# Performance work log

Hardware: AMD Instinct MI355X
Metric: run time of the kernel (lower is better)

Reference implementation:

```python
import jax, jax.numpy as jnp
import numpy as np
import math

B = 256          # batch size
D = 128          # input_size (embed dim)
N = 500000       # output_size == num_samples (memory bank rows)
K = 2048         # num_negative_samples
T = 0.07         # temperature
MOM = 0.5        # momentum
EPS = 1e-07


def _l2norm(x):
    return x / jnp.linalg.norm(x, axis=-1, keepdims=True)


def setup_inputs() -> dict:
    key = jax.random.key(0)
    k1, k2, k3, k4, k5, k6 = jax.random.split(key, 6)
    stdv = 1.0 / math.sqrt(D / 3.0)
    memory_v1 = jax.random.uniform(k1, (N, D), dtype=jnp.float32) * (2 * stdv) - stdv
    memory_v2 = jax.random.uniform(k2, (N, D), dtype=jnp.float32) * (2 * stdv) - stdv
    # embeds come out of an L2-normalization module in the original pipeline
    student_embed = _l2norm(jax.random.normal(k3, (B, D), dtype=jnp.float32))
    teacher_embed = _l2norm(jax.random.normal(k4, (B, D), dtype=jnp.float32))
    pos_idx = jax.random.randint(k5, (B,), 0, N, dtype=jnp.int64)
    contrast_idx = jax.random.randint(k6, (B, K + 1), 0, N, dtype=jnp.int64)
    contrast_idx = contrast_idx.at[:, 0].set(pos_idx)  # column 0 holds the positive
    return {
        'student_embed': student_embed,
        'teacher_embed': teacher_embed,
        'memory_v1': memory_v1,
        'memory_v2': memory_v2,
        'pos_idx': pos_idx,
        'contrast_idx': contrast_idx,
    }


def _contrast_loss(x):
    # x: [B, K+1] normalized exp-similarities; column 0 is the positive
    m = x.shape[1] - 1
    pn = 1.0 / float(N)  # num_samples
    noise = m * pn + EPS
    p_pos = x[:, 0]
    log_d1 = jnp.log(p_pos / (p_pos + noise))
    p_neg = x[:, 1:]
    log_d0 = jnp.log((m * pn) / (p_neg + noise))
    return -(log_d1.sum() + log_d0.sum()) / x.shape[0]


def reference(student_embed, teacher_embed, memory_v1, memory_v2, pos_idx, contrast_idx):
    output_size = memory_v1.shape[0]
    # gather [B, K+1, D] rows from each bank (detached in original)
    w1 = jax.lax.stop_gradient(memory_v1[contrast_idx])
    w2 = jax.lax.stop_gradient(memory_v2[contrast_idx])
    # per-sample bmm + exp/div  (teacher scored against v1 bank, student against v2)
    out_v2 = jnp.exp(jnp.einsum('bkd,bd->bk', w1, teacher_embed) / T)
    out_v1 = jnp.exp(jnp.einsum('bkd,bd->bk', w2, student_embed) / T)
    # first-call normalization constants (treated as constants thereafter)
    z_v1 = jax.lax.stop_gradient(out_v1.mean() * output_size)
    z_v2 = jax.lax.stop_gradient(out_v2.mean() * output_size)
    out_v1 = out_v1 / z_v1
    out_v2 = out_v2 / z_v2
    # momentum-weighted renormalize-and-scatter memory update (no_grad)
    s = jax.lax.stop_gradient(student_embed)
    t = jax.lax.stop_gradient(teacher_embed)
    l_pos = memory_v1[pos_idx] * MOM + s * (1.0 - MOM)
    updated_v1 = l_pos / jnp.sqrt((l_pos ** 2).sum(1, keepdims=True))
    new_memory_v1 = memory_v1.at[pos_idx].set(updated_v1)
    ab_pos = memory_v2[pos_idx] * MOM + t * (1.0 - MOM)
    updated_v2 = ab_pos / jnp.sqrt((ab_pos ** 2).sum(1, keepdims=True))
    new_memory_v2 = memory_v2.at[pos_idx].set(updated_v2)
    loss = _contrast_loss(out_v1) + _contrast_loss(out_v2)
    return loss, new_memory_v1, new_memory_v2
```

## Files before the change

### kernel.cpp

```cpp
#include <hip/hip_runtime.h>
#include <math.h>

namespace {
constexpr int kB = 256;
constexpr int kD = 128;
constexpr int kN = 500000;
constexpr int kKC = 2049;
constexpr int kNPair = kB * kKC;
constexpr float kTInv = 1.0f / 0.07f;
constexpr float kMom = 0.5f;
constexpr int kRB = 256;
constexpr long long kM = (long long)kN * kD;
constexpr long long kTot = 2 * kM;
constexpr int kChunk = 2048;
constexpr int kNB1 = (kN + kChunk - 1) / kChunk;
constexpr int kRows = 64;
constexpr int kTPB = (kN + kRows - 1) / kRows;
constexpr int kTiles = 2 * kTPB;
constexpr int kLdsStride = 132;
constexpr int kTilesPerBlock = 8;
constexpr int kGrid3 = (kTiles + kTilesPerBlock - 1) / kTilesPerBlock;
}


__global__ __launch_bounds__(256) void zero2_kernel(int* __restrict__ A, int* __restrict__ cur)
{
    int i = blockIdx.x * 256 + threadIdx.x;
    if (i < kN) { A[i] = 0; cur[i] = 0; }
}

__global__ __launch_bounds__(256) void hist_kernel(const int* __restrict__ cidx, int* __restrict__ A)
{
    int i = blockIdx.x * 256 + threadIdx.x;
    if (i < kNPair) atomicAdd(&A[cidx[i]], 1);
}

__global__ __launch_bounds__(256) void scan1_kernel(const int* __restrict__ A, int* __restrict__ bsum)
{
    long long base = (long long)blockIdx.x * kChunk;
    int t = threadIdx.x;
    int s = 0;
    #pragma unroll
    for (int j = 0; j < 8; ++j) {
        long long i = base + t * 8 + j;
        if (i < kN) s += A[i];
    }
    __shared__ int lds[256];
    lds[t] = s; __syncthreads();
    for (int st = 128; st > 0; st >>= 1) {
        if (t < st) lds[t] += lds[t + st];
        __syncthreads();
    }
    if (t == 0) bsum[blockIdx.x] = lds[0];
}

__global__ __launch_bounds__(256) void scan2_kernel(
    const int* __restrict__ bsum, int* __restrict__ bpre, int* __restrict__ offs)
{
    int t = threadIdx.x;
    int v = (t < kNB1) ? bsum[t] : 0;
    __shared__ int lds[256];
    lds[t] = v; __syncthreads();
    for (int st = 1; st < 256; st <<= 1) {
        int add = (t >= st) ? lds[t - st] : 0;
        __syncthreads();
        lds[t] += add;
        __syncthreads();
    }
    if (t < kNB1) bpre[t] = lds[t] - v;
    if (t == kNB1 - 1) offs[kN] = lds[t];
}

__global__ __launch_bounds__(256) void scan3_kernel(
    const int* __restrict__ A, const int* __restrict__ bpre, int* __restrict__ offs)
{
    int t = threadIdx.x;
    long long base = (long long)blockIdx.x * kChunk;
    int c[8]; int s = 0;
    #pragma unroll
    for (int j = 0; j < 8; ++j) {
        long long i = base + t * 8 + j;
        c[j] = (i < kN) ? A[i] : 0;
        s += c[j];
    }
    __shared__ int lds[256];
    lds[t] = s; __syncthreads();
    for (int st = 1; st < 256; st <<= 1) {
        int add = (t >= st) ? lds[t - st] : 0;
        __syncthreads();
        lds[t] += add;
        __syncthreads();
    }
    int excl = lds[t] - s + bpre[blockIdx.x];
    #pragma unroll
    for (int j = 0; j < 8; ++j) {
        long long i = base + t * 8 + j;
        if (i < kN) { offs[i] = excl; excl += c[j]; }
    }
}

__global__ __launch_bounds__(256) void scatter_kernel(
    const int* __restrict__ cidx, const int* __restrict__ offs,
    int* __restrict__ cur, int* __restrict__ sorted)
{
    int p = blockIdx.x * 256 + threadIdx.x;
    if (p < kNPair) {
        int r = cidx[p];
        int pos = offs[r] + atomicAdd(&cur[r], 1);
        sorted[pos] = p;
    }
}

__global__ __launch_bounds__(256) void fused3_kernel(
    const float* __restrict__ mem1, const float* __restrict__ mem2,
    const float* __restrict__ teacher, const float* __restrict__ student,
    const int* __restrict__ offs, const int* __restrict__ sorted,
    const int* __restrict__ cidx,
    float* __restrict__ out, float* __restrict__ e2, float* __restrict__ e1)
{
    __shared__ float tile[kRows * kLdsStride];
    const int tid = threadIdx.x;
    const int lane = tid & 63;
    const int w = tid >> 6;
    float4* ov = reinterpret_cast<float4*>(out);

    if (blockIdx.x == 0 && tid == 0) out[kTot] = mem2[kM - 1];

    int T0 = blockIdx.x * kTilesPerBlock;
    int T1 = T0 + kTilesPerBlock; if (T1 > kTiles) T1 = kTiles;
    for (int T = T0; T < T1; ++T) {
        int bk = (T >= kTPB) ? 1 : 0;
        int tt = T - bk * kTPB;
        int r0 = tt * kRows;
        int R  = kN - r0; if (R > kRows) R = kRows;

        if (w * 16 < R) {
            const float4* bank4 = reinterpret_cast<const float4*>(bk ? mem2 : mem1);
            long long chunk = (long long)r0 * kD + w * 2048;
            long long cb4   = chunk >> 2;
            long long base4 = (((long long)bk * kM) + chunk) >> 2;
            float4 v[8];
            #pragma unroll
            for (int i = 0; i < 8; ++i) v[i] = bank4[cb4 + i * 64 + lane];
            float carry = 0.f;
            long long gg = (long long)bk * kM + chunk - 1;
            if (gg >= 0) carry = (gg < kM) ? mem1[gg] : mem2[gg - kM];
            #pragma unroll
            for (int i = 0; i < 8; ++i) {
                float4 cur = v[i];
                int lr  = w * 16 + i * 2 + (lane >> 5);
                int col = (lane & 31) * 4;
                *reinterpret_cast<float4*>(&tile[lr * kLdsStride + col]) = cur;
                float pw = __shfl_up(cur.w, 1);
                if (lane == 0) pw = carry;
                carry = __shfl(cur.w, 63);
                long long k4 = base4 + i * 64 + lane;
                if (k4 != 0) {
                    ov[k4] = make_float4(pw, cur.x, cur.y, cur.z);
                } else {
                    out[1] = cur.x; out[2] = cur.y; out[3] = cur.z;
                }
            }
        }
        __syncthreads();

        int o0  = offs[r0];
        int cnt = offs[r0 + R] - o0;
        const float* emb = bk ? student : teacher;
        float* ep = bk ? e1 : e2;
        for (int t = tid; t < cnt; t += 256) {
            int p  = sorted[o0 + t];
            int lr = cidx[p] - r0;
            unsigned b = (unsigned)p / (unsigned)kKC;
            const float4* er = reinterpret_cast<const float4*>(emb + (long long)b * kD);
            const float* row = &tile[lr * kLdsStride];
            float ax = 0.f, ay = 0.f, az = 0.f, aw = 0.f;
            #pragma unroll 8
            for (int kk = 0; kk < 32; ++kk) {
                float4 rv = *reinterpret_cast<const float4*>(&row[kk * 4]);
                float4 ev = er[kk];
                ax += rv.x * ev.x; ay += rv.y * ev.y;
                az += rv.z * ev.z; aw += rv.w * ev.w;
            }
            ep[p] = __expf((ax + ay + az + aw) * kTInv);
        }
        __syncthreads();
    }
}


__global__ __launch_bounds__(256) void dots_kernel(
    const float* __restrict__ mem1, const float* __restrict__ mem2,
    const float* __restrict__ teacher, const float* __restrict__ student,
    const int* __restrict__ cidx,
    float* __restrict__ e2, float* __restrict__ e1)
{
    int gtid = blockIdx.x * 256 + threadIdx.x;
    int wave = gtid >> 6;
    int lane = threadIdx.x & 63;
    if (wave >= kNPair) return;
    int b = wave / kKC;
    long long row = (long long)cidx[wave] * kD;
    const float2 m1 = *reinterpret_cast<const float2*>(mem1 + row + lane * 2);
    const float2 m2 = *reinterpret_cast<const float2*>(mem2 + row + lane * 2);
    const float2 tv = *reinterpret_cast<const float2*>(teacher + b * kD + lane * 2);
    const float2 sv = *reinterpret_cast<const float2*>(student + b * kD + lane * 2);
    float d1 = m1.x * tv.x + m1.y * tv.y;
    float d2 = m2.x * sv.x + m2.y * sv.y;
    #pragma unroll
    for (int off = 32; off > 0; off >>= 1) {
        d1 += __shfl_xor(d1, off);
        d2 += __shfl_xor(d2, off);
    }
    if (lane == 0) {
        e2[wave] = __expf(d1 * kTInv);
        e1[wave] = __expf(d2 * kTInv);
    }
}

__global__ __launch_bounds__(256) void copy_kernel(
    const float* __restrict__ mem1, const float* __restrict__ mem2,
    float* __restrict__ out)
{
    const long long NV4 = (kTot + 1) / 4;
    const long long KS  = kM / 4;
    const float4* m1v = reinterpret_cast<const float4*>(mem1);
    const float4* m2v = reinterpret_cast<const float4*>(mem2);
    float4* ov = reinterpret_cast<float4*>(out);
    long long stride = (long long)gridDim.x * 256;
    for (long long k = (long long)blockIdx.x * 256 + threadIdx.x; k < NV4; k += stride) {
        if (k == 0) {
            out[1] = mem1[0]; out[2] = mem1[1]; out[3] = mem1[2];
            out[kTot] = mem2[kM - 1];
            continue;
        }
        float4 r;
        if (k < KS) {
            float4 a = m1v[k - 1];
            float4 b = m1v[k];
            r = make_float4(a.w, b.x, b.y, b.z);
        } else if (k == KS) {
            r = make_float4(mem1[kM - 1], mem2[0], mem2[1], mem2[2]);
        } else {
            float4 a = m2v[k - KS - 1];
            float4 b = m2v[k - KS];
            r = make_float4(a.w, b.x, b.y, b.z);
        }
        ov[k] = r;
    }
}


__global__ __launch_bounds__(256) void sums_kernel(
    const float* __restrict__ e2, const float* __restrict__ e1,
    float* __restrict__ p2, float* __restrict__ p1)
{
    __shared__ float s2[256], s1[256];
    float a2 = 0.f, a1 = 0.f;
    for (int i = blockIdx.x * 256 + threadIdx.x; i < kNPair; i += 256 * kRB) {
        a2 += e2[i];
        a1 += e1[i];
    }
    s2[threadIdx.x] = a2; s1[threadIdx.x] = a1;
    __syncthreads();
    for (int st = 128; st > 0; st >>= 1) {
        if ((int)threadIdx.x < st) {
            s2[threadIdx.x] += s2[threadIdx.x + st];
            s1[threadIdx.x] += s1[threadIdx.x + st];
        }
        __syncthreads();
    }
    if (threadIdx.x == 0) { p2[blockIdx.x] = s2[0]; p1[blockIdx.x] = s1[0]; }
}

__global__ __launch_bounds__(256) void z_kernel(
    const float* __restrict__ p2, const float* __restrict__ p1, float* __restrict__ z)
{
    __shared__ float s2[256], s1[256];
    s2[threadIdx.x] = p2[threadIdx.x];
    s1[threadIdx.x] = p1[threadIdx.x];
    __syncthreads();
    for (int st = 128; st > 0; st >>= 1) {
        if ((int)threadIdx.x < st) {
            s2[threadIdx.x] += s2[threadIdx.x + st];
            s1[threadIdx.x] += s1[threadIdx.x + st];
        }
        __syncthreads();
    }
    if (threadIdx.x == 0) {
        const float scale = (float)kN / (float)kNPair;
        z[0] = s2[0] * scale;
        z[1] = s1[0] * scale;
    }
}

__global__ __launch_bounds__(256) void lossp_kernel(
    const float* __restrict__ e2, const float* __restrict__ e1,
    const float* __restrict__ z, float* __restrict__ lp)
{
    const float mpn = 2048.0f / 500000.0f;
    const float noise = mpn + 1e-7f;
    const float iz2 = 1.0f / z[0];
    const float iz1 = 1.0f / z[1];
    float acc = 0.f;
    for (int i = blockIdx.x * 256 + threadIdx.x; i < kNPair; i += 256 * kRB) {
        int k = i % kKC;
        float x2 = e2[i] * iz2;
        float x1 = e1[i] * iz1;
        if (k == 0) {
            acc += __logf(x2 / (x2 + noise)) + __logf(x1 / (x1 + noise));
        } else {
            acc += __logf(mpn / (x2 + noise)) + __logf(mpn / (x1 + noise));
        }
    }
    __shared__ float s[256];
    s[threadIdx.x] = acc;
    __syncthreads();
    for (int st = 128; st > 0; st >>= 1) {
        if ((int)threadIdx.x < st) s[threadIdx.x] += s[threadIdx.x + st];
        __syncthreads();
    }
    if (threadIdx.x == 0) lp[blockIdx.x] = s[0];
}

__global__ __launch_bounds__(256) void final_kernel(
    const float* __restrict__ lp, float* __restrict__ out)
{
    __shared__ float s[256];
    s[threadIdx.x] = lp[threadIdx.x];
    __syncthreads();
    for (int st = 128; st > 0; st >>= 1) {
        if ((int)threadIdx.x < st) s[threadIdx.x] += s[threadIdx.x + st];
        __syncthreads();
    }
    if (threadIdx.x == 0) out[0] = -s[0] / (float)kB;
}


__global__ __launch_bounds__(64) void update_kernel(
    const float* __restrict__ mem1, const float* __restrict__ mem2,
    const float* __restrict__ student, const float* __restrict__ teacher,
    const int* __restrict__ pos_idx,
    float* __restrict__ out1, float* __restrict__ out2)
{
    int b = blockIdx.x;
    int lane = threadIdx.x;
    int p = pos_idx[b];
    for (int b2 = b + 1; b2 < kB; ++b2)
        if (pos_idx[b2] == p) return;
    long long row = (long long)p * kD;
    float2 m1 = *reinterpret_cast<const float2*>(mem1 + row + lane * 2);
    float2 m2 = *reinterpret_cast<const float2*>(mem2 + row + lane * 2);
    float2 sv = *reinterpret_cast<const float2*>(student + b * kD + lane * 2);
    float2 tv = *reinterpret_cast<const float2*>(teacher + b * kD + lane * 2);
    float2 l1 = make_float2(m1.x * kMom + sv.x * (1.f - kMom),
                            m1.y * kMom + sv.y * (1.f - kMom));
    float2 l2 = make_float2(m2.x * kMom + tv.x * (1.f - kMom),
                            m2.y * kMom + tv.y * (1.f - kMom));
    float n1 = l1.x * l1.x + l1.y * l1.y;
    float n2 = l2.x * l2.x + l2.y * l2.y;
    #pragma unroll
    for (int off = 32; off > 0; off >>= 1) {
        n1 += __shfl_xor(n1, off);
        n2 += __shfl_xor(n2, off);
    }
    float i1 = 1.0f / sqrtf(n1);
    float i2 = 1.0f / sqrtf(n2);
    out1[row + lane * 2]     = l1.x * i1;
    out1[row + lane * 2 + 1] = l1.y * i1;
    out2[row + lane * 2]     = l2.x * i2;
    out2[row + lane * 2 + 1] = l2.y * i2;
}

extern "C" void kernel_launch(void* const* d_in, const int* in_sizes, int n_in,
                              void* d_out, int out_size, void* d_ws, size_t ws_size,
                              hipStream_t stream) {
    const float* student = (const float*)d_in[0];
    const float* teacher = (const float*)d_in[1];
    const float* mem1    = (const float*)d_in[2];
    const float* mem2    = (const float*)d_in[3];
    const int*   pos_idx = (const int*)d_in[4];
    const int*   cidx    = (const int*)d_in[5];

    float* out  = (float*)d_out;
    float* out1 = out + 1;
    float* out2 = out + 1 + kM;

    float* ws = (float*)d_ws;
    float* e2 = ws;
    float* e1 = e2 + kNPair;
    float* p2 = e1 + kNPair;
    float* p1 = p2 + kRB;
    float* zz = p1 + kRB;
    float* lp = zz + 2;
    int*   A      = (int*)(lp + kRB);
    int*   cur    = A + kN;
    int*   offs   = cur + kN;
    int*   bsum   = offs + kN + 1;
    int*   bpre   = bsum + kNB1;
    int*   sorted = bpre + kNB1;
    size_t need = (size_t)((char*)(sorted + kNPair) - (char*)d_ws);

    if (ws_size >= need) {
        zero2_kernel<<<(kN + 255) / 256, 256, 0, stream>>>(A, cur);
        hist_kernel<<<(kNPair + 255) / 256, 256, 0, stream>>>(cidx, A);
        scan1_kernel<<<kNB1, 256, 0, stream>>>(A, bsum);
        scan2_kernel<<<1, 256, 0, stream>>>(bsum, bpre, offs);
        scan3_kernel<<<kNB1, 256, 0, stream>>>(A, bpre, offs);
        scatter_kernel<<<(kNPair + 255) / 256, 256, 0, stream>>>(cidx, offs, cur, sorted);
        fused3_kernel<<<kGrid3, 256, 0, stream>>>(mem1, mem2, teacher, student,
                                                  offs, sorted, cidx, out, e2, e1);
    } else {
        int nblocks = (kNPair + 3) / 4;
        dots_kernel<<<nblocks, 256, 0, stream>>>(mem1, mem2, teacher, student, cidx, e2, e1);
        copy_kernel<<<2048, 256, 0, stream>>>(mem1, mem2, out);
    }

    sums_kernel<<<kRB, 256, 0, stream>>>(e2, e1, p2, p1);
    z_kernel<<<1, 256, 0, stream>>>(p2, p1, zz);
    lossp_kernel<<<kRB, 256, 0, stream>>>(e2, e1, zz, lp);
    final_kernel<<<1, 256, 0, stream>>>(lp, out);
    update_kernel<<<kB, 64, 0, stream>>>(mem1, mem2, student, teacher, pos_idx, out1, out2);
}
```

Measured before the change: 329.7 us.

## Make fused copy-and-dot kernel wave-independent with register double-buffered segment prefetch

The block-wide 64-row tiles shared by four waves are replaced by per-wave 16-row segments, each in its own LDS slice. The __syncthreads barriers are removed, and each wave now handles 8 consecutive segments. The next segment's bank data is loaded into registers while the current one is copied out and scored, so global loads overlap with the dot-product phase. This costs more registers per thread, and per-segment work can become unbalanced when few indices hit a segment.

New measurement: 361.4 us. 1.1x slower.

```diff
diff --git a/kernel.cpp b/kernel.cpp
--- a/kernel.cpp
+++ b/kernel.cpp
@@ -14,12 +14,14 @@
 constexpr long long kTot = 2 * kM;
 constexpr int kChunk = 2048;
 constexpr int kNB1 = (kN + kChunk - 1) / kChunk;
-constexpr int kRows = 64;
-constexpr int kTPB = (kN + kRows - 1) / kRows;
-constexpr int kTiles = 2 * kTPB;
 constexpr int kLdsStride = 132;
-constexpr int kTilesPerBlock = 8;
-constexpr int kGrid3 = (kTiles + kTilesPerBlock - 1) / kTilesPerBlock;
+constexpr int kSegRows = 16;
+constexpr int kSegFloats = kSegRows * kD;
+constexpr int kSegs = (int)(kTot / kSegFloats);
+constexpr int kSegsB1 = kSegs / 2;
+constexpr int kSPW = 8;
+constexpr int kWaves5 = (kSegs + kSPW - 1) / kSPW;
+constexpr int kBlocks5 = (kWaves5 + 3) / 4;
 }
 
 
@@ -111,69 +113,84 @@
     }
 }
 
-__global__ __launch_bounds__(256) void fused3_kernel(
+__global__ __launch_bounds__(256) void fused5_kernel(
     const float* __restrict__ mem1, const float* __restrict__ mem2,
     const float* __restrict__ teacher, const float* __restrict__ student,
     const int* __restrict__ offs, const int* __restrict__ sorted,
     const int* __restrict__ cidx,
     float* __restrict__ out, float* __restrict__ e2, float* __restrict__ e1)
 {
-    __shared__ float tile[kRows * kLdsStride];
+    __shared__ float tile[4][kSegRows * kLdsStride];
     const int tid = threadIdx.x;
     const int lane = tid & 63;
     const int w = tid >> 6;
+    float* my = tile[w];
+
+    long long gw = (long long)blockIdx.x * 4 + w;
+    long long s0 = gw * kSPW;
+    if (s0 >= kSegs) return;
+    long long s1 = s0 + kSPW; if (s1 > kSegs) s1 = kSegs;
+
     float4* ov = reinterpret_cast<float4*>(out);
-
-    if (blockIdx.x == 0 && tid == 0) out[kTot] = mem2[kM - 1];
-
-    int T0 = blockIdx.x * kTilesPerBlock;
-    int T1 = T0 + kTilesPerBlock; if (T1 > kTiles) T1 = kTiles;
-    for (int T = T0; T < T1; ++T) {
-        int bk = (T >= kTPB) ? 1 : 0;
-        int tt = T - bk * kTPB;
-        int r0 = tt * kRows;
-        int R  = kN - r0; if (R > kRows) R = kRows;
-
-        if (w * 16 < R) {
-            const float4* bank4 = reinterpret_cast<const float4*>(bk ? mem2 : mem1);
-            long long chunk = (long long)r0 * kD + w * 2048;
-            long long cb4   = chunk >> 2;
-            long long base4 = (((long long)bk * kM) + chunk) >> 2;
-            float4 v[8];
+    const float4* m1v = reinterpret_cast<const float4*>(mem1);
+    const float4* m2v = reinterpret_cast<const float4*>(mem2);
+
+    if (gw == 0 && lane == 0) out[kTot] = mem2[kM - 1];
+
+    float carry = 0.f;
+    if (s0 > 0) {
+        long long g = s0 * kSegFloats - 1;
+        carry = (g < kM) ? mem1[g] : mem2[g - kM];
+    }
+
+    float4 va[8];
+    {
+        bool b1 = (s0 < kSegsB1);
+        long long lb4 = (b1 ? s0 : s0 - kSegsB1) * 8 * 64;
+        const float4* bp = b1 ? m1v : m2v;
+        #pragma unroll
+        for (int i = 0; i < 8; ++i) va[i] = bp[lb4 + i * 64 + lane];
+    }
+
+    for (long long s = s0; s < s1; ++s) {
+        float4 vb[8];
+        if (s + 1 < s1) {
+            bool nb1 = (s + 1 < kSegsB1);
+            long long lb4 = (nb1 ? (s + 1) : (s + 1 - kSegsB1)) * 8 * 64;
+            const float4* bp = nb1 ? m1v : m2v;
             #pragma unroll
-            for (int i = 0; i < 8; ++i) v[i] = bank4[cb4 + i * 64 + lane];
-            float carry = 0.f;
-            long long gg = (long long)bk * kM + chunk - 1;
-            if (gg >= 0) carry = (gg < kM) ? mem1[gg] : mem2[gg - kM];
-            #pragma unroll
-            for (int i = 0; i < 8; ++i) {
-                float4 cur = v[i];
-                int lr  = w * 16 + i * 2 + (lane >> 5);
-                int col = (lane & 31) * 4;
-                *reinterpret_cast<float4*>(&tile[lr * kLdsStride + col]) = cur;
-                float pw = __shfl_up(cur.w, 1);
-                if (lane == 0) pw = carry;
-                carry = __shfl(cur.w, 63);
-                long long k4 = base4 + i * 64 + lane;
-                if (k4 != 0) {
-                    ov[k4] = make_float4(pw, cur.x, cur.y, cur.z);
-                } else {
-                    out[1] = cur.x; out[2] = cur.y; out[3] = cur.z;
-                }
+            for (int i = 0; i < 8; ++i) vb[i] = bp[lb4 + i * 64 + lane];
+        }
+
+        long long j0 = s * 8;
+        #pragma unroll
+        for (int i = 0; i < 8; ++i) {
+            float4 cur = va[i];
+            int lr = i * 2 + (lane >> 5);
+            *reinterpret_cast<float4*>(&my[lr * kLdsStride + (lane & 31) * 4]) = cur;
+            float pw = __shfl_up(cur.w, 1);
+            if (lane == 0) pw = carry;
+            carry = __shfl(cur.w, 63);
+            long long k4 = (j0 + i) * 64 + lane;
+            if (k4 != 0) {
+                ov[k4] = make_float4(pw, cur.x, cur.y, cur.z);
+            } else {
+                out[1] = cur.x; out[2] = cur.y; out[3] = cur.z;
             }
         }
-        __syncthreads();
-
+
+        bool b1 = (s < kSegsB1);
+        int r0 = (int)((b1 ? s : s - kSegsB1) * kSegRows);
         int o0  = offs[r0];
-        int cnt = offs[r0 + R] - o0;
-        const float* emb = bk ? student : teacher;
-        float* ep = bk ? e1 : e2;
-        for (int t = tid; t < cnt; t += 256) {
+        int cnt = offs[r0 + kSegRows] - o0;
+        const float* emb = b1 ? teacher : student;
+        float* ep = b1 ? e2 : e1;
+        for (int t = lane; t < cnt; t += 64) {
             int p  = sorted[o0 + t];
             int lr = cidx[p] - r0;
-            unsigned b = (unsigned)p / (unsigned)kKC;
-            const float4* er = reinterpret_cast<const float4*>(emb + (long long)b * kD);
-            const float* row = &tile[lr * kLdsStride];
+            unsigned bb = (unsigned)p / (unsigned)kKC;
+            const float4* er = reinterpret_cast<const float4*>(emb + (long long)bb * kD);
+            const float* row = &my[lr * kLdsStride];
             float ax = 0.f, ay = 0.f, az = 0.f, aw = 0.f;
             #pragma unroll 8
             for (int kk = 0; kk < 32; ++kk) {
@@ -184,7 +201,9 @@
             }
             ep[p] = __expf((ax + ay + az + aw) * kTInv);
         }
-        __syncthreads();
+
+        #pragma unroll
+        for (int i = 0; i < 8; ++i) va[i] = vb[i];
     }
 }
 
@@ -408,8 +427,8 @@
         scan2_kernel<<<1, 256, 0, stream>>>(bsum, bpre, offs);
         scan3_kernel<<<kNB1, 256, 0, stream>>>(A, bpre, offs);
         scatter_kernel<<<(kNPair + 255) / 256, 256, 0, stream>>>(cidx, offs, cur, sorted);
-        fused3_kernel<<<kGrid3, 256, 0, stream>>>(mem1, mem2, teacher, student,
-                                                  offs, sorted, cidx, out, e2, e1);
+        fused5_kernel<<<kBlocks5, 256, 0, stream>>>(mem1, mem2, teacher, student,
+                                                    offs, sorted, cidx, out, e2, e1);
     } else {
         int nblocks = (kNPair + 3) / 4;
         dots_kernel<<<nblocks, 256, 0, stream>>>(mem1, mem2, teacher, student, cidx, e2, e1);
```

## Prefetch next tile's bank rows into registers while processing current tile

Applied to the files above, without the earlier changes.

The fused copy+dot kernel now double-buffers the global loads of the memory-bank tile. Loads for the next tile are issued into a second register array before the current tile is written to LDS and scored, so memory latency can overlap compute. The __syncthreads calls become explicit s_barrier plus sched_barrier so the compiler keeps the early loads. Out-of-range loads are clamped and stores are masked instead of skipping whole waves. This doubles the register footprint of the staging buffers, which may reduce occupancy.

New measurement: 396.0 us. +20.1%, slower.

```diff
diff --git a/kernel.cpp b/kernel.cpp
--- a/kernel.cpp
+++ b/kernel.cpp
@@ -19,7 +19,7 @@
 constexpr int kTiles = 2 * kTPB;
 constexpr int kLdsStride = 132;
 constexpr int kTilesPerBlock = 8;
-constexpr int kGrid3 = (kTiles + kTilesPerBlock - 1) / kTilesPerBlock;
+constexpr int kGrid6 = (kTiles + kTilesPerBlock - 1) / kTilesPerBlock;
 }
 
 
@@ -111,7 +111,7 @@
     }
 }
 
-__global__ __launch_bounds__(256) void fused3_kernel(
+__global__ __launch_bounds__(256) void fused6_kernel(
     const float* __restrict__ mem1, const float* __restrict__ mem2,
     const float* __restrict__ teacher, const float* __restrict__ student,
     const int* __restrict__ offs, const int* __restrict__ sorted,
@@ -126,43 +126,59 @@
 
     if (blockIdx.x == 0 && tid == 0) out[kTot] = mem2[kM - 1];
 
-    int T0 = blockIdx.x * kTilesPerBlock;
+    const int T0 = blockIdx.x * kTilesPerBlock;
     int T1 = T0 + kTilesPerBlock; if (T1 > kTiles) T1 = kTiles;
-    for (int T = T0; T < T1; ++T) {
+
+    auto issue = [&](float4 (&v)[8], int T) {
         int bk = (T >= kTPB) ? 1 : 0;
         int tt = T - bk * kTPB;
-        int r0 = tt * kRows;
-        int R  = kN - r0; if (R > kRows) R = kRows;
-
-        if (w * 16 < R) {
-            const float4* bank4 = reinterpret_cast<const float4*>(bk ? mem2 : mem1);
-            long long chunk = (long long)r0 * kD + w * 2048;
-            long long cb4   = chunk >> 2;
-            long long base4 = (((long long)bk * kM) + chunk) >> 2;
-            float4 v[8];
-            #pragma unroll
-            for (int i = 0; i < 8; ++i) v[i] = bank4[cb4 + i * 64 + lane];
-            float carry = 0.f;
-            long long gg = (long long)bk * kM + chunk - 1;
-            if (gg >= 0) carry = (gg < kM) ? mem1[gg] : mem2[gg - kM];
-            #pragma unroll
-            for (int i = 0; i < 8; ++i) {
-                float4 cur = v[i];
-                int lr  = w * 16 + i * 2 + (lane >> 5);
-                int col = (lane & 31) * 4;
-                *reinterpret_cast<float4*>(&tile[lr * kLdsStride + col]) = cur;
-                float pw = __shfl_up(cur.w, 1);
-                if (lane == 0) pw = carry;
-                carry = __shfl(cur.w, 63);
-                long long k4 = base4 + i * 64 + lane;
+        const float4* bank4 = reinterpret_cast<const float4*>(bk ? mem2 : mem1);
+        long long cb4 = ((long long)tt * kRows * kD + w * 2048) >> 2;
+        const long long maxv4 = kM / 4 - 1;
+        #pragma unroll
+        for (int i = 0; i < 8; ++i) {
+            long long e4 = cb4 + i * 64 + lane;
+            if (e4 > maxv4) e4 = maxv4;
+            v[i] = bank4[e4];
+        }
+    };
+
+    auto body = [&](float4 (&v)[8], float4 (&nxt)[8], int T, bool hasNext) {
+        if (hasNext) issue(nxt, T + 1);
+        __builtin_amdgcn_sched_barrier(0);
+
+        int bk = (T >= kTPB) ? 1 : 0;
+        int tt = T - bk * kTPB;
+        long long r0 = (long long)tt * kRows;
+        int R = (int)((kN - r0 < kRows) ? (kN - r0) : kRows);
+        long long gbase = (long long)bk * kM + r0 * kD + w * 2048;
+
+        float carry = 0.f;
+        if (gbase > 0) {
+            long long g = gbase - 1;
+            carry = (g < kM) ? mem1[g] : mem2[g - kM];
+        }
+        bool fullw = (w * 16 + 15) < R;
+        #pragma unroll
+        for (int i = 0; i < 8; ++i) {
+            float4 c = v[i];
+            int lr = w * 16 + i * 2 + (lane >> 5);
+            *reinterpret_cast<float4*>(&tile[lr * kLdsStride + (lane & 31) * 4]) = c;
+            float pw = __shfl_up(c.w, 1);
+            if (lane == 0) pw = carry;
+            carry = __shfl(c.w, 63);
+            long long k4 = (gbase >> 2) + i * 64 + lane;
+            if (fullw || (r0 + lr) < kN) {
                 if (k4 != 0) {
-                    ov[k4] = make_float4(pw, cur.x, cur.y, cur.z);
+                    ov[k4] = make_float4(pw, c.x, c.y, c.z);
                 } else {
-                    out[1] = cur.x; out[2] = cur.y; out[3] = cur.z;
+                    out[1] = c.x; out[2] = c.y; out[3] = c.z;
                 }
             }
         }
-        __syncthreads();
+        asm volatile("s_waitcnt lgkmcnt(0)" ::: "memory");
+        __builtin_amdgcn_s_barrier();
+        __builtin_amdgcn_sched_barrier(0);
 
         int o0  = offs[r0];
         int cnt = offs[r0 + R] - o0;
@@ -170,9 +186,9 @@
         float* ep = bk ? e1 : e2;
         for (int t = tid; t < cnt; t += 256) {
             int p  = sorted[o0 + t];
-            int lr = cidx[p] - r0;
-            unsigned b = (unsigned)p / (unsigned)kKC;
-            const float4* er = reinterpret_cast<const float4*>(emb + (long long)b * kD);
+            int lr = cidx[p] - (int)r0;
+            unsigned bb = (unsigned)p / (unsigned)kKC;
+            const float4* er = reinterpret_cast<const float4*>(emb + (long long)bb * kD);
             const float* row = &tile[lr * kLdsStride];
             float ax = 0.f, ay = 0.f, az = 0.f, aw = 0.f;
             #pragma unroll 8
@@ -184,7 +200,16 @@
             }
             ep[p] = __expf((ax + ay + az + aw) * kTInv);
         }
-        __syncthreads();
+        __builtin_amdgcn_sched_barrier(0);
+        __builtin_amdgcn_s_barrier();
+        __builtin_amdgcn_sched_barrier(0);
+    };
+
+    float4 va[8], vb[8];
+    issue(va, T0);
+    for (int T = T0; T < T1; T += 2) {
+        body(va, vb, T, T + 1 < T1);
+        if (T + 1 < T1) body(vb, va, T + 1, T + 2 < T1);
     }
 }
 
@@ -408,7 +433,7 @@
         scan2_kernel<<<1, 256, 0, stream>>>(bsum, bpre, offs);
         scan3_kernel<<<kNB1, 256, 0, stream>>>(A, bpre, offs);
         scatter_kernel<<<(kNPair + 255) / 256, 256, 0, stream>>>(cidx, offs, cur, sorted);
-        fused3_kernel<<<kGrid3, 256, 0, stream>>>(mem1, mem2, teacher, student,
+        fused6_kernel<<<kGrid6, 256, 0, stream>>>(mem1, mem2, teacher, student,
                                                   offs, sorted, cidx, out, e2, e1);
     } else {
         int nblocks = (kNPair + 3) / 4;
```
